# Optimization experiments

Hardware: AMD Instinct MI355X
Metric: run time of the kernel (lower is better)

Reference implementation:

```python
import jax, jax.numpy as jnp
from jax import lax
import numpy as np

D = 512        # d_model
F = 128        # raw feature dim
MS = 1024      # logic (service) nodes
NP_ = 16384    # physical nodes
EL = 4096      # logic edges
EP = 131072    # phys edges
SRC = 0        # source_node_idx
NEG = -1e9


def _gnn(feats, edge_index, Win, Wout, N):
    row, col = edge_index
    h = jax.nn.relu(feats @ Win)                                  # [N, D]
    agg = jax.ops.segment_sum(h[row], col, num_segments=N)        # [N, D]
    return jax.nn.relu((h + agg) @ Wout)


def _bfs_hop(edge_index, N, src, iters=16):
    # BFS hop distance from src (bounded Bellman-Ford relaxation)
    row, col = edge_index
    big = jnp.int32(N)
    dist = jnp.full((N,), big, jnp.int32).at[src].set(0)
    def body(_, d):
        cand = jnp.minimum(d[row] + 1, big)
        upd = jax.ops.segment_min(cand, col, num_segments=N)
        return jnp.minimum(d, upd)
    return lax.fori_loop(0, iters, body, dist)


def _forward(logic_feats, phys_feats, Ws_in, Ws_out, Wp_in, Wp_out,
             sA1, sA2, pA1, pA2, Wq, Wk, Wc1, bc1, wc2,
             logic_edge_index, phys_edge_index, actions, static_mask, topo_order):
    Np = phys_feats.shape[0]
    cloud = Np - 1                                                # cloud_node_idx = -1
    h_s = _gnn(logic_feats, logic_edge_index, Ws_in, Ws_out, logic_feats.shape[0])
    h_p = _gnn(phys_feats, phys_edge_index, Wp_in, Wp_out, Np)
    # task-specific residual adapters
    h_s = h_s + jax.nn.relu(h_s @ sA1) @ sA2
    h_p = h_p + jax.nn.relu(h_p @ pA1) @ pA2
    metric = _bfs_hop(phys_edge_index, Np, SRC)                   # [Np] int32
    q_all = (h_s @ Wq) / jnp.sqrt(jnp.float32(D))                 # [Ms, D]
    K = h_p @ Wk                                                  # [Np, D]
    acts = actions.astype(jnp.int32)

    def step(state, i):
        visited, last, logp_sum, ent_sum, switches, relax = state
        base = static_mask[i]                                     # [Np] bool
        # cloud_sticky branch
        sticky = jnp.zeros_like(base).at[cloud].set(base[cloud])
        # forbid_return (allow_stay keeps `last`)
        forbid = visited.at[last].set(False)
        allowed_n = base & (~forbid) & (metric >= metric[last])   # metric_non_decreasing
        allowed = jnp.where(last == cloud, sticky, allowed_n)
        any_a = allowed.any()
        # relaxation fallback: stay -> cloud -> base
        fb_stay = jnp.zeros_like(base).at[last].set(True)
        fb_cloud = jnp.zeros_like(base).at[cloud].set(True)
        fallback = jnp.where(base[last], fb_stay, jnp.where(base[cloud], fb_cloud, base))
        allowed = jnp.where(any_a, allowed, fallback)
        # actor: masked categorical over physical nodes
        logits = K @ q_all[i]                                     # [Np]
        logp_all = jax.nn.log_softmax(jnp.where(allowed, logits, NEG))
        p = jnp.exp(logp_all)
        ent = -jnp.sum(p * logp_all)
        a = acts[i]
        ne = a != last
        visited = visited.at[last].set(visited[last] | ne)
        last = jnp.where(ne, a, last)
        return (visited, last, logp_sum + logp_all[a], ent_sum + ent,
                switches + ne.astype(jnp.int32), relax + (~any_a).astype(jnp.int32)), None

    init = (jnp.zeros((Np,), bool), jnp.int32(SRC),
            jnp.float32(0.0), jnp.float32(0.0), jnp.int32(0), jnp.int32(0))
    (visited, last, logp_sum, ent_sum, switches, relax), _ = lax.scan(
        step, init, topo_order.astype(jnp.int32))
    # value head
    pooled = jnp.concatenate([h_s.mean(0), h_p.mean(0)])          # [2D]
    value = jax.nn.relu(pooled @ Wc1 + bc1) @ wc2                 # scalar
    return jnp.stack([logp_sum, ent_sum, value])


def setup_inputs() -> dict:
    key = jax.random.key(0)
    ks = jax.random.split(key, 20)
    s = 0.05
    def w(k, shape):
        return jax.random.normal(k, shape, jnp.float32) * s
    return {
        "logic_edge_index": jax.random.randint(ks[0], (2, EL), 0, MS, jnp.int32),
        "logic_feats": jax.random.normal(ks[1], (MS, F), jnp.float32),
        "phys_edge_index": jax.random.randint(ks[2], (2, EP), 0, NP_, jnp.int32),
        "phys_feats": jax.random.normal(ks[3], (NP_, F), jnp.float32),
        "actions": jax.random.randint(ks[4], (MS,), 0, NP_, jnp.int32),
        "static_mask": jnp.ones((MS, NP_), bool),
        "topo_order": jnp.arange(MS, dtype=jnp.int32),
        "Ws_in": w(ks[5], (F, D)), "Ws_out": w(ks[6], (D, D)),
        "Wp_in": w(ks[7], (F, D)), "Wp_out": w(ks[8], (D, D)),
        "sA1": w(ks[9], (D, D)), "sA2": w(ks[10], (D, D)),
        "pA1": w(ks[11], (D, D)), "pA2": w(ks[12], (D, D)),
        "Wq": w(ks[13], (D, D)), "Wk": w(ks[14], (D, D)),
        "Wc1": w(ks[15], (2 * D, D)),
        "bc1": jnp.zeros((D,), jnp.float32),
        "wc2": w(ks[16], (D,)),
    }


def reference(logic_edge_index, logic_feats, phys_edge_index, phys_feats,
              actions, static_mask, topo_order,
              Ws_in, Ws_out, Wp_in, Wp_out, sA1, sA2, pA1, pA2,
              Wq, Wk, Wc1, bc1, wc2):
    return _forward(logic_feats, phys_feats, Ws_in, Ws_out, Wp_in, Wp_out,
                    sA1, sA2, pA1, pA2, Wq, Wk, Wc1, bc1, wc2,
                    logic_edge_index, phys_edge_index, actions, static_mask, topo_order)
```

## Files before the change

### kernel.cpp

```cpp
#include <hip/hip_runtime.h>
#include <cstdint>
#include <cstddef>

typedef __bf16 bf16_t;
typedef uint8_t u8;
typedef u8 u8x4v __attribute__((ext_vector_type(4)));
typedef float f32x4 __attribute__((ext_vector_type(4)));

#define NEGV (-1e9f)

#define GLDS(gp, lp) __builtin_amdgcn_global_load_lds( \
    (const __attribute__((address_space(1))) void*)(gp), \
    (__attribute__((address_space(3))) void*)(lp), 16, 0, 0)

template<int SEL>
__device__ inline float fp8decw(uint32_t w) { return __builtin_amdgcn_cvt_f32_fp8((int)w, SEL); }
__device__ inline float fp8dec(u8 b) { return __builtin_amdgcn_cvt_f32_fp8((int)b, 0); }
__device__ inline u8 f2fp8(float x) {
    return (u8)(__builtin_amdgcn_cvt_pk_fp8_f32(x, x, 0, false) & 0xFF);
}

struct PrepArgs {
    const float* w512src[8]; u8* w512dst[8];
    const float* w128src[2]; u8* w128dst[2];
    const float* logicF; const float* physF;
    u8* featsSb; u8* featsPb;
    const int* mask; uint32_t* bits;
    int* cntC; int* cntR; int* cntL; int* firstL; int* dist;
    float* pooled; float* hacc;
};

__global__ __launch_bounds__(256)
void k_prep(PrepArgs p) {
    __shared__ float tb[64][65];
    const int b = blockIdx.x, tid = threadIdx.x;
    if (b < 544) {
        const float* src; u8* dst; int K, tile;
        if (b < 512) { src = p.w512src[b >> 6]; dst = p.w512dst[b >> 6]; K = 512; tile = b & 63; }
        else { int bb = b - 512; src = p.w128src[bb >> 4]; dst = p.w128dst[bb >> 4]; K = 128; tile = bb & 15; }
        const int N = 512;
        int kt = tile >> 3, tc = tile & 7;
        int cx = tid & 63, ry = tid >> 6;
#pragma unroll
        for (int q = 0; q < 16; ++q) {
            int r = q * 4 + ry;
            tb[r][cx] = src[(size_t)(kt * 64 + r) * N + tc * 64 + cx];
        }
        __syncthreads();
#pragma unroll
        for (int q = 0; q < 16; ++q) {
            int r2 = q * 4 + ry;
            dst[(size_t)(tc * 64 + r2) * K + kt * 64 + cx] = f2fp8(tb[cx][r2]);
        }
    } else if (b < 672) {
        size_t e0 = (size_t)(b - 544) * 1024 + tid * 4;
        float4 v = *(const float4*)(p.logicF + e0);
        int pk = __builtin_amdgcn_cvt_pk_fp8_f32(v.x, v.y, 0, false);
        pk = __builtin_amdgcn_cvt_pk_fp8_f32(v.z, v.w, pk, true);
        *(uint32_t*)(p.featsSb + e0) = (uint32_t)pk;
    } else if (b < 2720) {
        size_t e0 = (size_t)(b - 672) * 1024 + tid * 4;
        float4 v = *(const float4*)(p.physF + e0);
        int pk = __builtin_amdgcn_cvt_pk_fp8_f32(v.x, v.y, 0, false);
        pk = __builtin_amdgcn_cvt_pk_fp8_f32(v.z, v.w, pk, true);
        *(uint32_t*)(p.featsPb + e0) = (uint32_t)pk;
    } else if (b < 2784) {
        int gid = (b - 2720) * 256 + tid;
        p.cntC[gid] = 0; p.cntR[gid] = 0; p.firstL[gid] = 0x7fffffff;
        p.dist[gid] = (gid == 0) ? 0 : 16384;
        if (gid < 1024) { p.cntL[gid] = 0; p.pooled[gid] = 0.0f; }
        if (gid < 512) p.hacc[gid] = 0.0f;
    } else {
        size_t w = (size_t)(b - 2784) * 256 + tid;
        const int4* q4 = (const int4*)(p.mask + w * 32);
        uint32_t bb = 0;
#pragma unroll
        for (int q = 0; q < 8; ++q) {
            int4 v = q4[q];
            bb |= (v.x != 0 ? 1u : 0u) << (q * 4);
            bb |= (v.y != 0 ? 1u : 0u) << (q * 4 + 1);
            bb |= (v.z != 0 ? 1u : 0u) << (q * 4 + 2);
            bb |= (v.w != 0 ? 1u : 0u) << (q * 4 + 3);
        }
        p.bits[w] = bb;
    }
}

__global__ void k_hist3(const int* __restrict__ rowP, const int* __restrict__ colP,
                        const int* __restrict__ rowL, const int* __restrict__ colL,
                        int* cntC, int* cntR, int* cntL, int EP, int EL,
                        const int* __restrict__ topo, const int* __restrict__ acts,
                        int* __restrict__ lastArr, int* __restrict__ firstL) {
    int b = blockIdx.x;
    if (b < 1040) {
        int e = b * 256 + threadIdx.x;
        if (e < EP) atomicAdd(&cntC[colP[e]], 1);
        else if (e < 2 * EP) atomicAdd(&cntR[rowP[e - EP]], 1);
        else if (e < 2 * EP + EL) atomicAdd(&cntL[colL[e - 2 * EP]], 1);
    } else {
        int s = (b - 1040) * 256 + threadIdx.x;
        int last = (s == 0) ? 0 : acts[topo[s - 1]];
        lastArr[s] = last;
        int a = acts[topo[s]];
        if (a != last) atomicMin(&firstL[last], s);
    }
}

__global__ __launch_bounds__(256)
void k_scan3(int* cntC, int* offC, int* curC,
             int* cntR, int* offR, int* curR,
             int* cntL, int* offL, int* curL) {
    __shared__ int ss[256];
    const int tid = threadIdx.x;
    if (blockIdx.x < 2) {
        int* cnt; int* off; int* cur;
        if (blockIdx.x == 0) { cnt = cntC; off = offC; cur = curC; }
        else                 { cnt = cntR; off = offR; cur = curR; }
        int4 v[16];
        const int4* pv = (const int4*)(cnt + tid * 64);
#pragma unroll
        for (int i = 0; i < 16; ++i) v[i] = pv[i];
        int s = 0;
#pragma unroll
        for (int i = 0; i < 16; ++i) s += v[i].x + v[i].y + v[i].z + v[i].w;
        ss[tid] = s; __syncthreads();
        for (int d = 1; d < 256; d <<= 1) {
            int t = (tid >= d) ? ss[tid - d] : 0;
            __syncthreads(); ss[tid] += t; __syncthreads();
        }
        int run = (tid == 0) ? 0 : ss[tid - 1];
        int4* po = (int4*)(off + tid * 64);
        int4* pc = (int4*)(cur + tid * 64);
#pragma unroll
        for (int i = 0; i < 16; ++i) {
            int4 o;
            o.x = run; run += v[i].x;
            o.y = run; run += v[i].y;
            o.z = run; run += v[i].z;
            o.w = run; run += v[i].w;
            po[i] = o; pc[i] = o;
        }
        if (tid == 255) off[16384] = run;
    } else {
        int4 v = *(const int4*)(cntL + tid * 4);
        int s = v.x + v.y + v.z + v.w;
        ss[tid] = s; __syncthreads();
        for (int d = 1; d < 256; d <<= 1) {
            int t = (tid >= d) ? ss[tid - d] : 0;
            __syncthreads(); ss[tid] += t; __syncthreads();
        }
        int run = (tid == 0) ? 0 : ss[tid - 1];
        int4 o;
        o.x = run; run += v.x;
        o.y = run; run += v.y;
        o.z = run; run += v.z;
        o.w = run; run += v.w;
        *(int4*)(offL + tid * 4) = o;
        *(int4*)(curL + tid * 4) = o;
        if (tid == 255) offL[1024] = run;
    }
}

__global__ void k_scatter3(const int* __restrict__ rowP, const int* __restrict__ colP,
                           const int* __restrict__ rowL, const int* __restrict__ colL,
                           int* curC, int* curR, int* curL,
                           int* erowCP, int* ecolRP, int* erowL, int EP, int EL) {
    int e = blockIdx.x * 256 + threadIdx.x;
    if (e < EP) {
        int c = colP[e]; int q = atomicAdd(&curC[c], 1); erowCP[q] = rowP[e];
    } else if (e < 2 * EP) {
        int e2 = e - EP;
        int c = rowP[e2]; int q = atomicAdd(&curR[c], 1); ecolRP[q] = colP[e2];
    } else if (e < 2 * EP + EL) {
        int e3 = e - 2 * EP;
        int c = colL[e3]; int q = atomicAdd(&curL[c], 1); erowL[q] = rowL[e3];
    }
}

__global__ __launch_bounds__(256)
void k_bfs_level(const int* __restrict__ offR, const int* __restrict__ ecol,
                 int* __restrict__ dist, int lev) {
    int j = blockIdx.x * 256 + threadIdx.x;
    if (dist[j] != lev) return;
    int e0 = offR[j], e1 = offR[j + 1];
    for (int e = e0; e < e1; ++e) {
        int v = ecol[e];
        if (dist[v] == 16384) dist[v] = lev + 1;
    }
}

__global__ __launch_bounds__(256)
void k_fmpack(const int* __restrict__ firstL, const int* __restrict__ dist, int* __restrict__ fm) {
    int j = blockIdx.x * 256 + threadIdx.x;
    int fl = firstL[j]; if (fl > 0xFFFF) fl = 0xFFFF;
    fm[j] = (fl << 16) | dist[j];
}

struct GemmDesc { const u8* A; const u8* B; const u8* Cin; void* O;
                  int N; int K; float scale; int relu; int obf; };
struct GemmPair { GemmDesc d0; GemmDesc d1; int split; };

__global__ __launch_bounds__(256)
void gemm_mfma(GemmPair args) {
    __shared__ u8 As[2][128 * 64];
    __shared__ u8 Bs[2][128 * 64];
    const int nwg = gridDim.x * gridDim.y;
    const int cpx = nwg >> 3;
    const int pfl = blockIdx.y * gridDim.x + blockIdx.x;
    const int vfl = (pfl & 7) * cpx + (pfl >> 3);
    const int vbx = vfl % gridDim.x;
    const int vby = vfl / gridDim.x;
    const int inSet1 = (vby >= args.split);
    const GemmDesc g = inSet1 ? args.d1 : args.d0;
    const int my = vby - (inSet1 ? args.split : 0);
    const int m0 = my * 128, n0 = vbx * 128;
    const int tid = threadIdx.x, wave = tid >> 6, lane = tid & 63;
    const int wm = (wave >> 1) * 64, wn = (wave & 1) * 64;
    const int lr = lane & 15, lkq = lane >> 4;
    const int K = g.K;
    const int srr = wave * 16 + (lane >> 2);
    const int scb = (((lane & 3) ^ ((lane >> 2) & 3)) << 4);
    const u8* Abase = g.A + (size_t)(m0 + srr) * K + scb;
    const u8* Bbase = g.B + (size_t)(n0 + srr) * K + scb;
    const size_t rstep = (size_t)64 * K;
    f32x4 acc[4][4] = {};

    auto stage = [&](int q, int k0) {
        GLDS(Abase + k0,         &As[q][(wave * 16) * 64]);
        GLDS(Abase + k0 + rstep, &As[q][(64 + wave * 16) * 64]);
        GLDS(Bbase + k0,         &Bs[q][(wave * 16) * 64]);
        GLDS(Bbase + k0 + rstep, &Bs[q][(64 + wave * 16) * 64]);
    };

    stage(0, 0);
    asm volatile("s_waitcnt vmcnt(0)" ::: "memory");
    __syncthreads();
    const int nt = K >> 6;
    for (int t = 0; t < nt; ++t) {
        int cur = t & 1;
        if (t + 1 < nt) stage(cur ^ 1, (t + 1) << 6);
#pragma unroll
        for (int kh = 0; kh < 2; ++kh) {
            long af[4], bf[4];
#pragma unroll
            for (int mi = 0; mi < 4; ++mi) {
                int r = wm + mi * 16 + lr;
                int pb = r * 64 + ((kh * 32 + lkq * 8) ^ ((r & 3) << 4));
                af[mi] = *(const long*)&As[cur][pb];
            }
#pragma unroll
            for (int ni = 0; ni < 4; ++ni) {
                int r = wn + ni * 16 + lr;
                int pb = r * 64 + ((kh * 32 + lkq * 8) ^ ((r & 3) << 4));
                bf[ni] = *(const long*)&Bs[cur][pb];
            }
#pragma unroll
            for (int mi = 0; mi < 4; ++mi)
#pragma unroll
                for (int ni = 0; ni < 4; ++ni)
                    acc[mi][ni] = __builtin_amdgcn_mfma_f32_16x16x32_fp8_fp8(af[mi], bf[ni], acc[mi][ni], 0, 0, 0);
        }
        asm volatile("s_waitcnt vmcnt(0)" ::: "memory");
        __syncthreads();
    }
    const int rb = m0 + wm + (lane >> 4) * 4;
    const int cb = n0 + wn + lr;
#pragma unroll
    for (int mi = 0; mi < 4; ++mi)
#pragma unroll
        for (int ni = 0; ni < 4; ++ni)
#pragma unroll
            for (int r = 0; r < 4; ++r) {
                int row = rb + mi * 16 + r;
                int col = cb + ni * 16;
                size_t idx = (size_t)row * g.N + col;
                float v = acc[mi][ni][r] * g.scale;
                if (g.Cin) v += fp8dec(g.Cin[idx]);
                if (g.relu) v = fmaxf(v, 0.0f);
                if (g.obf) ((bf16_t*)g.O)[idx] = (bf16_t)v;
                else       ((u8*)g.O)[idx] = f2fp8(v);
            }
}

__global__ __launch_bounds__(256)
void k_spmm2(const u8* __restrict__ HL, const int* __restrict__ offL, const int* __restrict__ erowL, u8* __restrict__ XL,
             const u8* __restrict__ HP, const int* __restrict__ offP, const int* __restrict__ erowP, u8* __restrict__ XP) {
    int b = blockIdx.x;
    const u8* H; const int* off; const int* erow; u8* X; int c;
    int wib = threadIdx.x >> 6, lane = threadIdx.x & 63;
    if (b < 256) { H = HL; off = offL; erow = erowL; X = XL; c = b * 4 + wib; }
    else { b -= 256; H = HP; off = offP; erow = erowP; X = XP; c = b * 4 + wib; }
    int d0 = lane * 8;
    float acc[8] = {0,0,0,0,0,0,0,0};
    int e0 = off[c], e1 = off[c + 1];
    for (int e = e0; e < e1; ++e) {
        int r = erow[e];
        uint2 w = *(const uint2*)(H + (size_t)r * 512 + d0);
        acc[0] += fp8decw<0>(w.x);
        acc[1] += fp8decw<1>(w.x);
        acc[2] += fp8decw<2>(w.x);
        acc[3] += fp8decw<3>(w.x);
        acc[4] += fp8decw<0>(w.y);
        acc[5] += fp8decw<1>(w.y);
        acc[6] += fp8decw<2>(w.y);
        acc[7] += fp8decw<3>(w.y);
    }
    uint2 ow = *(const uint2*)(H + (size_t)c * 512 + d0);
    float o0 = fp8decw<0>(ow.x) + acc[0];
    float o1 = fp8decw<1>(ow.x) + acc[1];
    float o2 = fp8decw<2>(ow.x) + acc[2];
    float o3 = fp8decw<3>(ow.x) + acc[3];
    float o4 = fp8decw<0>(ow.y) + acc[4];
    float o5 = fp8decw<1>(ow.y) + acc[5];
    float o6 = fp8decw<2>(ow.y) + acc[6];
    float o7 = fp8decw<3>(ow.y) + acc[7];
    int lo = __builtin_amdgcn_cvt_pk_fp8_f32(o0, o1, 0, false);
    lo = __builtin_amdgcn_cvt_pk_fp8_f32(o2, o3, lo, true);
    int hi = __builtin_amdgcn_cvt_pk_fp8_f32(o4, o5, 0, false);
    hi = __builtin_amdgcn_cvt_pk_fp8_f32(o6, o7, hi, true);
    uint2 res; res.x = (uint32_t)lo; res.y = (uint32_t)hi;
    *(uint2*)(X + (size_t)c * 512 + d0) = res;
}

__global__ __launch_bounds__(256)
void k_scan2(const bf16_t* __restrict__ S, const uint32_t* __restrict__ bits,
             const int* __restrict__ fm, const int* __restrict__ topo,
             const int* __restrict__ acts, const int* __restrict__ lastA,
             float* __restrict__ slogp, float* __restrict__ sent) {
    typedef bf16_t bf16x8 __attribute__((ext_vector_type(8)));
    const int NPn = 16384, cloud = NPn - 1;
    __shared__ float msh[256], zsh[256], wsh[256];
    __shared__ int ash[256];
    const int s = blockIdx.x, tid = threadIdx.x;
    const int i = topo[s], a = acts[i], last = lastA[s];
    const bf16_t* Srow = S + (size_t)i * NPn;
    const uint32_t* brow = bits + (size_t)i * 512;
    const int ml = fm[last] & 0xFFFF;
    const int baseCloud = (brow[511] >> 31) & 1;
    const int lic = (last == cloud);
    if (lic && baseCloud) {
        if (tid == 0) {
            float M = (float)Srow[cloud];
            slogp[s] = (a == cloud) ? 0.0f : (NEGV - M);
            sent[s] = 0.0f;
        }
        return;
    }
    float m = -3.4e38f, Z = 0.0f, W = 0.0f;
    int any = 0;
    if (!lic) {
        for (int c = 0; c < 8; ++c) {
            int j0 = c * 2048 + tid * 8;
            bf16x8 sv = *(const bf16x8*)(Srow + j0);
            uint32_t b8 = (brow[j0 >> 5] >> (j0 & 24)) & 0xFFu;
            int4 f0 = *(const int4*)(fm + j0);
            int4 f1 = *(const int4*)(fm + j0 + 4);
            int fj[8] = {f0.x, f0.y, f0.z, f0.w, f1.x, f1.y, f1.z, f1.w};
#pragma unroll
            for (int q = 0; q < 8; ++q) {
                int j = j0 + q;
                bool alw = ((b8 >> q) & 1) && ((fj[q] & 0xFFFF) >= ml)
                           && (j == last || (((unsigned)fj[q]) >> 16) >= (unsigned)s);
                if (alw) {
                    any = 1;
                    float l = (float)sv[q];
                    if (l > m) {
                        float d = m - l, ce = expf(d);
                        W = ce * (W + d * Z);
                        Z = ce * Z + 1.0f;
                        m = l;
                    } else {
                        float t = l - m, e = expf(t);
                        Z += e; W += t * e;
                    }
                }
            }
        }
    }
    msh[tid] = m; zsh[tid] = Z; wsh[tid] = W; ash[tid] = any;
    __syncthreads();
    for (int st = 128; st > 0; st >>= 1) {
        if (tid < st) {
            float m1 = msh[tid], Z1 = zsh[tid], W1 = wsh[tid];
            float m2 = msh[tid + st], Z2 = zsh[tid + st], W2 = wsh[tid + st];
            float M2 = fmaxf(m1, m2);
            float e1 = expf(m1 - M2), e2 = expf(m2 - M2);
            zsh[tid] = e1 * Z1 + e2 * Z2;
            wsh[tid] = e1 * (W1 + (m1 - M2) * Z1) + e2 * (W2 + (m2 - M2) * Z2);
            msh[tid] = M2;
            ash[tid] |= ash[tid + st];
        }
        __syncthreads();
    }
    if (tid != 0) return;
    if (ash[0]) {
        float M = msh[0], Zt = zsh[0], Wt = wsh[0];
        float logZ = logf(Zt);
        int fa = fm[a];
        bool alwa = ((brow[a >> 5] >> (a & 31)) & 1) && ((fa & 0xFFFF) >= ml)
                    && (a == last || (((unsigned)fa) >> 16) >= (unsigned)s);
        float la = alwa ? (float)Srow[a] : NEGV;
        slogp[s] = la - M - logZ;
        sent[s] = logZ - Wt / Zt;
        return;
    }
    int baseLast = (brow[last >> 5] >> (last & 31)) & 1;
    if (baseLast) { float M = (float)Srow[last]; slogp[s] = (a == last) ? 0.0f : (NEGV - M); sent[s] = 0.0f; return; }
    if (baseCloud) { float M = (float)Srow[cloud]; slogp[s] = (a == cloud) ? 0.0f : (NEGV - M); sent[s] = 0.0f; return; }
    float mm = -3.4e38f, ZZ = 0.0f, WW = 0.0f;
    for (int j = 0; j < NPn; ++j) {
        if ((brow[j >> 5] >> (j & 31)) & 1) {
            float l = (float)Srow[j];
            if (l > mm) { float d = mm - l, ce = expf(d); WW = ce * (WW + d * ZZ); ZZ = ce * ZZ + 1.0f; mm = l; }
            else { float t = l - mm, e = expf(t); ZZ += e; WW += t * e; }
        }
    }
    if (ZZ == 0.0f) { slogp[s] = -logf((float)NPn); sent[s] = logf((float)NPn); return; }
    float logZ = logf(ZZ);
    int ba = (brow[a >> 5] >> (a & 31)) & 1;
    float la = ba ? (float)Srow[a] : NEGV;
    slogp[s] = la - mm - logZ;
    sent[s] = logZ - WW / ZZ;
}

__global__ __launch_bounds__(256)
void k_pool2(const u8* __restrict__ HL, const u8* __restrict__ HP, float* __restrict__ pooled) {
    int b = blockIdx.x, tid = threadIdx.x;
    const u8* H; float* dst; int R, bb, ng; float inv;
    if (b < 16) { H = HL; dst = pooled; R = 1024; inv = 1.0f / 1024.0f; bb = b; ng = 16; }
    else { H = HP; dst = pooled + 512; R = 16384; inv = 1.0f / 16384.0f; bb = b - 16; ng = 128; }
    int c0 = tid * 2;
    float a0 = 0, a1 = 0;
    for (int r = bb; r < R; r += ng) {
        uint32_t w = *(const unsigned short*)(H + (size_t)r * 512 + c0);
        a0 += fp8decw<0>(w);
        a1 += fp8decw<1>(w);
    }
    atomicAdd(&dst[c0], a0 * inv);
    atomicAdd(&dst[c0 + 1], a1 * inv);
}

__global__ __launch_bounds__(256)
void k_vpart(const float* __restrict__ pooled, const float* __restrict__ Wc1, float* __restrict__ hacc) {
    __shared__ float pk[128];
    int b = blockIdx.x, tid = threadIdx.x;
    int k0 = b * 128;
    if (tid < 128) pk[tid] = pooled[k0 + tid];
    __syncthreads();
    float a0 = 0, a1 = 0;
    for (int kk = 0; kk < 128; ++kk) {
        float pv = pk[kk];
        const float* wr = Wc1 + (size_t)(k0 + kk) * 512;
        a0 += pv * wr[tid];
        a1 += pv * wr[tid + 256];
    }
    atomicAdd(&hacc[tid], a0);
    atomicAdd(&hacc[tid + 256], a1);
}

__global__ __launch_bounds__(256)
void k_epilogue(const float* __restrict__ slogp, const float* __restrict__ sent,
                const float* __restrict__ hacc, const float* __restrict__ bc1,
                const float* __restrict__ wc2, float* __restrict__ out) {
    __shared__ float s1[256], s2[256], s3[256];
    int tid = threadIdx.x;
    float a = 0, b = 0;
    for (int k = tid; k < 1024; k += 256) { a += slogp[k]; b += sent[k]; }
    float v = fmaxf(hacc[tid] + bc1[tid], 0.0f) * wc2[tid]
            + fmaxf(hacc[tid + 256] + bc1[tid + 256], 0.0f) * wc2[tid + 256];
    s1[tid] = a; s2[tid] = b; s3[tid] = v;
    __syncthreads();
    for (int st = 128; st > 0; st >>= 1) {
        if (tid < st) { s1[tid] += s1[tid + st]; s2[tid] += s2[tid + st]; s3[tid] += s3[tid + st]; }
        __syncthreads();
    }
    if (tid == 0) { out[0] = s1[0]; out[1] = s2[0]; out[2] = s3[0]; }
}

extern "C" void kernel_launch(void* const* d_in, const int* in_sizes, int n_in,
                              void* d_out, int out_size, void* d_ws, size_t ws_size,
                              hipStream_t stream) {
    (void)n_in; (void)out_size; (void)ws_size; (void)in_sizes;
    const int MS = 1024, NP = 16384, EL = 4096, EP = 131072, D = 512;

    const int* logicE = (const int*)d_in[0];
    const float* logicF = (const float*)d_in[1];
    const int* physE = (const int*)d_in[2];
    const float* physF = (const float*)d_in[3];
    const int* acts = (const int*)d_in[4];
    const int* mask = (const int*)d_in[5];
    const int* topo = (const int*)d_in[6];
    const float* Ws_in = (const float*)d_in[7];
    const float* Ws_out = (const float*)d_in[8];
    const float* Wp_in = (const float*)d_in[9];
    const float* Wp_out = (const float*)d_in[10];
    const float* sA1 = (const float*)d_in[11];
    const float* sA2 = (const float*)d_in[12];
    const float* pA1 = (const float*)d_in[13];
    const float* pA2 = (const float*)d_in[14];
    const float* Wq = (const float*)d_in[15];
    const float* Wk = (const float*)d_in[16];
    const float* Wc1 = (const float*)d_in[17];
    const float* bc1 = (const float*)d_in[18];
    const float* wc2 = (const float*)d_in[19];
    float* out = (float*)d_out;

    char* wsb = (char*)d_ws;
    size_t off = 0;
    auto alloc = [&](size_t bytes) -> void* {
        off = (off + 255) & ~(size_t)255;
        void* p = wsb + off; off += bytes; return p;
    };

    bf16_t* S_bf  = (bf16_t*)alloc((size_t)MS * NP * 2);
    u8* PB0     = (u8*)alloc((size_t)NP * D);
    u8* PB1     = (u8*)alloc((size_t)NP * D);
    u8* PB2     = (u8*)alloc((size_t)NP * D);
    u8* LB0     = (u8*)alloc((size_t)MS * D);
    u8* LB1     = (u8*)alloc((size_t)MS * D);
    u8* LB2     = (u8*)alloc((size_t)MS * D);
    u8* featsSb = (u8*)alloc((size_t)MS * 128);
    u8* featsPb = (u8*)alloc((size_t)NP * 128);
    u8* WsinT   = (u8*)alloc(512 * 128);
    u8* WpinT   = (u8*)alloc(512 * 128);
    u8* WsoutT  = (u8*)alloc(512 * 512);
    u8* sA1T    = (u8*)alloc(512 * 512);
    u8* sA2T    = (u8*)alloc(512 * 512);
    u8* WqT     = (u8*)alloc(512 * 512);
    u8* WpoutT  = (u8*)alloc(512 * 512);
    u8* pA1T    = (u8*)alloc(512 * 512);
    u8* pA2T    = (u8*)alloc(512 * 512);
    u8* WkT     = (u8*)alloc(512 * 512);
    uint32_t* bits = (uint32_t*)alloc((size_t)MS * NP / 8);
    int* cntC  = (int*)alloc(NP * 4);
    int* offC  = (int*)alloc((NP + 1) * 4);
    int* curC  = (int*)alloc(NP * 4);
    int* cntR  = (int*)alloc(NP * 4);
    int* offR  = (int*)alloc((NP + 1) * 4);
    int* curR  = (int*)alloc(NP * 4);
    int* cntL  = (int*)alloc(MS * 4);
    int* offL  = (int*)alloc((MS + 1) * 4);
    int* curL  = (int*)alloc(MS * 4);
    int* erowCP = (int*)alloc(EP * 4);
    int* ecolRP = (int*)alloc(EP * 4);
    int* erowL  = (int*)alloc(EL * 4);
    int* firstL = (int*)alloc(NP * 4);
    int* lastA  = (int*)alloc(MS * 4);
    int* dist   = (int*)alloc(NP * 4);
    int* fm     = (int*)alloc(NP * 4);
    float* slogp = (float*)alloc(MS * 4);
    float* sentb = (float*)alloc(MS * 4);
    float* pooled = (float*)alloc(1024 * 4);
    float* hacc   = (float*)alloc(512 * 4);

    const int* rowP = physE;  const int* colP = physE + EP;
    const int* rowL = logicE; const int* colL = logicE + EL;

    {
        PrepArgs p;
        const float* s512[8] = {Ws_out, sA1, sA2, Wq, Wp_out, pA1, pA2, Wk};
        u8* d512[8] = {WsoutT, sA1T, sA2T, WqT, WpoutT, pA1T, pA2T, WkT};
        for (int q = 0; q < 8; ++q) { p.w512src[q] = s512[q]; p.w512dst[q] = d512[q]; }
        p.w128src[0] = Ws_in; p.w128dst[0] = WsinT;
        p.w128src[1] = Wp_in; p.w128dst[1] = WpinT;
        p.logicF = logicF; p.physF = physF; p.featsSb = featsSb; p.featsPb = featsPb;
        p.mask = mask; p.bits = bits;
        p.cntC = cntC; p.cntR = cntR; p.cntL = cntL; p.firstL = firstL; p.dist = dist;
        p.pooled = pooled; p.hacc = hacc;
        hipLaunchKernelGGL(k_prep, dim3(4832), dim3(256), 0, stream, p);
    }
    hipLaunchKernelGGL(k_hist3, dim3(1044), dim3(256), 0, stream,
                       rowP, colP, rowL, colL, cntC, cntR, cntL, EP, EL,
                       topo, acts, lastA, firstL);
    hipLaunchKernelGGL(k_scan3, dim3(3), dim3(256), 0, stream,
                       cntC, offC, curC, cntR, offR, curR, cntL, offL, curL);
    hipLaunchKernelGGL(k_scatter3, dim3((2 * EP + EL) / 256), dim3(256), 0, stream,
                       rowP, colP, rowL, colL, curC, curR, curL, erowCP, ecolRP, erowL, EP, EL);
    for (int lev = 0; lev < 16; ++lev)
        hipLaunchKernelGGL(k_bfs_level, dim3(64), dim3(256), 0, stream, offR, ecolRP, dist, lev);
    hipLaunchKernelGGL(k_fmpack, dim3(64), dim3(256), 0, stream, firstL, dist, fm);

    auto gemm2 = [&](const u8* A0, const u8* B0, const u8* C0, void* O0, float sc0,
                     const u8* A1, const u8* B1, const u8* C1, void* O1, float sc1,
                     int K, int relu) {
        GemmPair gp;
        gp.d0 = {A0, B0, C0, O0, 512, K, sc0, relu, 0};
        gp.d1 = {A1, B1, C1, O1, 512, K, sc1, relu, 0};
        gp.split = 8;
        hipLaunchKernelGGL(gemm_mfma, dim3(4, 136), dim3(256), 0, stream, gp);
    };

    gemm2(featsSb, WsinT, nullptr, LB0, 1.0f, featsPb, WpinT, nullptr, PB0, 1.0f, 128, 1);
    hipLaunchKernelGGL(k_spmm2, dim3(256 + 4096), dim3(256), 0, stream,
                       LB0, offL, erowL, LB1, PB0, offC, erowCP, PB1);
    gemm2(LB1, WsoutT, nullptr, LB0, 1.0f, PB1, WpoutT, nullptr, PB0, 1.0f, 512, 1);
    gemm2(LB0, sA1T, nullptr, LB1, 1.0f, PB0, pA1T, nullptr, PB1, 1.0f, 512, 1);
    gemm2(LB1, sA2T, LB0, LB2, 1.0f, PB1, pA2T, PB0, PB2, 1.0f, 512, 0);
    hipLaunchKernelGGL(k_pool2, dim3(144), dim3(256), 0, stream, LB2, PB2, pooled);
    gemm2(LB2, WqT, nullptr, LB1, 0.044194173824159216f, PB2, WkT, nullptr, PB1, 1.0f, 512, 0);
    {
        GemmPair gp;
        gp.d0 = {LB1, PB1, nullptr, S_bf, NP, 512, 1.0f, 0, 1};
        gp.d1 = gp.d0;
        gp.split = 1000;
        hipLaunchKernelGGL(gemm_mfma, dim3(128, 8), dim3(256), 0, stream, gp);
    }
    hipLaunchKernelGGL(k_scan2, dim3(MS), dim3(256), 0, stream,
                       S_bf, bits, fm, topo, acts, lastA, slogp, sentb);
    hipLaunchKernelGGL(k_vpart, dim3(8), dim3(256), 0, stream, pooled, Wc1, hacc);
    hipLaunchKernelGGL(k_epilogue, dim3(1), dim3(256), 0, stream, slogp, sentb, hacc, bc1, wc2, out);
}
```

Before: 349.8 us.

## Fold BFS levels into GEMM, SpMM and pool launches as extra blocks

Levels 7 through 14 of the BFS relaxation no longer run as separate tiny kernels. Each one rides as 64 extra blocks at the front of an existing GEMM, SpMM or pool launch. The GEMM kernel now takes a 1D grid with explicit gx and nwg values for the tile swizzle. This removes about eight small serial launches and their gaps, and the BFS work overlaps with independent compute. In exchange, every GEMM block does extra index handling, and the BFS blocks compete for CUs during the main kernels.

```diff
diff --git a/kernel.cpp b/kernel.cpp
--- a/kernel.cpp
+++ b/kernel.cpp
@@ -4,7 +4,6 @@
 
 typedef __bf16 bf16_t;
 typedef uint8_t u8;
-typedef u8 u8x4v __attribute__((ext_vector_type(4)));
 typedef float f32x4 __attribute__((ext_vector_type(4)));
 
 #define NEGV (-1e9f)
@@ -18,6 +17,17 @@
 __device__ inline float fp8dec(u8 b) { return __builtin_amdgcn_cvt_f32_fp8((int)b, 0); }
 __device__ inline u8 f2fp8(float x) {
     return (u8)(__builtin_amdgcn_cvt_pk_fp8_f32(x, x, 0, false) & 0xFF);
+}
+
+__device__ inline void bfs_level_work(const int* __restrict__ offR, const int* __restrict__ ecol,
+                                      int* __restrict__ dist, int lev, int blk, int tid) {
+    int j = blk * 256 + tid;
+    if (dist[j] != lev) return;
+    int e0 = offR[j], e1 = offR[j + 1];
+    for (int e = e0; e < e1; ++e) {
+        int v = ecol[e];
+        if (dist[v] == 16384) dist[v] = lev + 1;
+    }
 }
 
 struct PrepArgs {
@@ -180,13 +190,7 @@
 __global__ __launch_bounds__(256)
 void k_bfs_level(const int* __restrict__ offR, const int* __restrict__ ecol,
                  int* __restrict__ dist, int lev) {
-    int j = blockIdx.x * 256 + threadIdx.x;
-    if (dist[j] != lev) return;
-    int e0 = offR[j], e1 = offR[j + 1];
-    for (int e = e0; e < e1; ++e) {
-        int v = ecol[e];
-        if (dist[v] == 16384) dist[v] = lev + 1;
-    }
+    bfs_level_work(offR, ecol, dist, lev, blockIdx.x, threadIdx.x);
 }
 
 __global__ __launch_bounds__(256)
@@ -198,23 +202,29 @@
 
 struct GemmDesc { const u8* A; const u8* B; const u8* Cin; void* O;
                   int N; int K; float scale; int relu; int obf; };
-struct GemmPair { GemmDesc d0; GemmDesc d1; int split; };
+struct GemmPair { GemmDesc d0; GemmDesc d1; int split; int gx; int nwg;
+                  const int* offR; const int* ecol; int* dist; int bfsLev; };
 
 __global__ __launch_bounds__(256)
 void gemm_mfma(GemmPair args) {
     __shared__ u8 As[2][128 * 64];
     __shared__ u8 Bs[2][128 * 64];
-    const int nwg = gridDim.x * gridDim.y;
-    const int cpx = nwg >> 3;
-    const int pfl = blockIdx.y * gridDim.x + blockIdx.x;
-    const int vfl = (pfl & 7) * cpx + (pfl >> 3);
-    const int vbx = vfl % gridDim.x;
-    const int vby = vfl / gridDim.x;
+    const int tid = threadIdx.x;
+    int f = blockIdx.x;
+    if (f < 64) {
+        bfs_level_work(args.offR, args.ecol, args.dist, args.bfsLev, f, tid);
+        return;
+    }
+    f -= 64;
+    const int cpx = args.nwg >> 3;
+    const int vfl = (f & 7) * cpx + (f >> 3);
+    const int vbx = vfl % args.gx;
+    const int vby = vfl / args.gx;
     const int inSet1 = (vby >= args.split);
     const GemmDesc g = inSet1 ? args.d1 : args.d0;
     const int my = vby - (inSet1 ? args.split : 0);
     const int m0 = my * 128, n0 = vbx * 128;
-    const int tid = threadIdx.x, wave = tid >> 6, lane = tid & 63;
+    const int wave = tid >> 6, lane = tid & 63;
     const int wm = (wave >> 1) * 64, wn = (wave & 1) * 64;
     const int lr = lane & 15, lkq = lane >> 4;
     const int K = g.K;
@@ -284,8 +294,11 @@
 
 __global__ __launch_bounds__(256)
 void k_spmm2(const u8* __restrict__ HL, const int* __restrict__ offL, const int* __restrict__ erowL, u8* __restrict__ XL,
-             const u8* __restrict__ HP, const int* __restrict__ offP, const int* __restrict__ erowP, u8* __restrict__ XP) {
+             const u8* __restrict__ HP, const int* __restrict__ offP, const int* __restrict__ erowP, u8* __restrict__ XP,
+             const int* __restrict__ offR, const int* __restrict__ ecol, int* __restrict__ dist, int bfsLev) {
     int b = blockIdx.x;
+    if (b < 64) { bfs_level_work(offR, ecol, dist, bfsLev, b, threadIdx.x); return; }
+    b -= 64;
     const u8* H; const int* off; const int* erow; u8* X; int c;
     int wib = threadIdx.x >> 6, lane = threadIdx.x & 63;
     if (b < 256) { H = HL; off = offL; erow = erowL; X = XL; c = b * 4 + wib; }
@@ -424,8 +437,11 @@
 }
 
 __global__ __launch_bounds__(256)
-void k_pool2(const u8* __restrict__ HL, const u8* __restrict__ HP, float* __restrict__ pooled) {
+void k_pool2(const u8* __restrict__ HL, const u8* __restrict__ HP, float* __restrict__ pooled,
+             const int* __restrict__ offR, const int* __restrict__ ecol, int* __restrict__ dist, int bfsLev) {
     int b = blockIdx.x, tid = threadIdx.x;
+    if (b < 64) { bfs_level_work(offR, ecol, dist, bfsLev, b, tid); return; }
+    b -= 64;
     const u8* H; float* dst; int R, bb, ng; float inv;
     if (b < 16) { H = HL; dst = pooled; R = 1024; inv = 1.0f / 1024.0f; bb = b; ng = 16; }
     else { H = HP; dst = pooled + 512; R = 16384; inv = 1.0f / 16384.0f; bb = b - 16; ng = 128; }
@@ -576,35 +592,40 @@
                        cntC, offC, curC, cntR, offR, curR, cntL, offL, curL);
     hipLaunchKernelGGL(k_scatter3, dim3((2 * EP + EL) / 256), dim3(256), 0, stream,
                        rowP, colP, rowL, colL, curC, curR, curL, erowCP, ecolRP, erowL, EP, EL);
-    for (int lev = 0; lev < 16; ++lev)
+    for (int lev = 0; lev < 7; ++lev)
         hipLaunchKernelGGL(k_bfs_level, dim3(64), dim3(256), 0, stream, offR, ecolRP, dist, lev);
-    hipLaunchKernelGGL(k_fmpack, dim3(64), dim3(256), 0, stream, firstL, dist, fm);
 
     auto gemm2 = [&](const u8* A0, const u8* B0, const u8* C0, void* O0, float sc0,
                      const u8* A1, const u8* B1, const u8* C1, void* O1, float sc1,
-                     int K, int relu) {
+                     int K, int relu, int bfsLev) {
         GemmPair gp;
         gp.d0 = {A0, B0, C0, O0, 512, K, sc0, relu, 0};
         gp.d1 = {A1, B1, C1, O1, 512, K, sc1, relu, 0};
-        gp.split = 8;
-        hipLaunchKernelGGL(gemm_mfma, dim3(4, 136), dim3(256), 0, stream, gp);
+        gp.split = 8; gp.gx = 4; gp.nwg = 544;
+        gp.offR = offR; gp.ecol = ecolRP; gp.dist = dist; gp.bfsLev = bfsLev;
+        hipLaunchKernelGGL(gemm_mfma, dim3(64 + 544), dim3(256), 0, stream, gp);
     };
 
-    gemm2(featsSb, WsinT, nullptr, LB0, 1.0f, featsPb, WpinT, nullptr, PB0, 1.0f, 128, 1);
-    hipLaunchKernelGGL(k_spmm2, dim3(256 + 4096), dim3(256), 0, stream,
-                       LB0, offL, erowL, LB1, PB0, offC, erowCP, PB1);
-    gemm2(LB1, WsoutT, nullptr, LB0, 1.0f, PB1, WpoutT, nullptr, PB0, 1.0f, 512, 1);
-    gemm2(LB0, sA1T, nullptr, LB1, 1.0f, PB0, pA1T, nullptr, PB1, 1.0f, 512, 1);
-    gemm2(LB1, sA2T, LB0, LB2, 1.0f, PB1, pA2T, PB0, PB2, 1.0f, 512, 0);
-    hipLaunchKernelGGL(k_pool2, dim3(144), dim3(256), 0, stream, LB2, PB2, pooled);
-    gemm2(LB2, WqT, nullptr, LB1, 0.044194173824159216f, PB2, WkT, nullptr, PB1, 1.0f, 512, 0);
+    gemm2(featsSb, WsinT, nullptr, LB0, 1.0f, featsPb, WpinT, nullptr, PB0, 1.0f, 128, 1, 7);
+    hipLaunchKernelGGL(k_spmm2, dim3(64 + 256 + 4096), dim3(256), 0, stream,
+                       LB0, offL, erowL, LB1, PB0, offC, erowCP, PB1,
+                       offR, ecolRP, dist, 8);
+    gemm2(LB1, WsoutT, nullptr, LB0, 1.0f, PB1, WpoutT, nullptr, PB0, 1.0f, 512, 1, 9);
+    gemm2(LB0, sA1T, nullptr, LB1, 1.0f, PB0, pA1T, nullptr, PB1, 1.0f, 512, 1, 10);
+    gemm2(LB1, sA2T, LB0, LB2, 1.0f, PB1, pA2T, PB0, PB2, 1.0f, 512, 0, 11);
+    hipLaunchKernelGGL(k_pool2, dim3(64 + 144), dim3(256), 0, stream, LB2, PB2, pooled,
+                       offR, ecolRP, dist, 12);
+    gemm2(LB2, WqT, nullptr, LB1, 0.044194173824159216f, PB2, WkT, nullptr, PB1, 1.0f, 512, 0, 13);
     {
         GemmPair gp;
         gp.d0 = {LB1, PB1, nullptr, S_bf, NP, 512, 1.0f, 0, 1};
         gp.d1 = gp.d0;
-        gp.split = 1000;
-        hipLaunchKernelGGL(gemm_mfma, dim3(128, 8), dim3(256), 0, stream, gp);
-    }
+        gp.split = 1000; gp.gx = 128; gp.nwg = 1024;
+        gp.offR = offR; gp.ecol = ecolRP; gp.dist = dist; gp.bfsLev = 14;
+        hipLaunchKernelGGL(gemm_mfma, dim3(64 + 1024), dim3(256), 0, stream, gp);
+    }
+    hipLaunchKernelGGL(k_bfs_level, dim3(64), dim3(256), 0, stream, offR, ecolRP, dist, 15);
+    hipLaunchKernelGGL(k_fmpack, dim3(64), dim3(256), 0, stream, firstL, dist, fm);
     hipLaunchKernelGGL(k_scan2, dim3(MS), dim3(256), 0, stream,
                        S_bf, bits, fm, topo, acts, lastA, slogp, sentb);
     hipLaunchKernelGGL(k_vpart, dim3(8), dim3(256), 0, stream, pooled, Wc1, hacc);
```

After: 337.3 us (median of 2 runs). 1.04x faster.
